# Kernel optimization log

Hardware: AMD Instinct MI355X
Metric: run time of the kernel (lower is better)

## Reference

```python
import jax, jax.numpy as jnp
import numpy as np
import math

N, DIM, HEADS = 4096, 128, 8
HC = DIM // HEADS      # MHA per-head dim = 16
GC = DIM               # TransformerConv per-head out_channels = dim (concat=False)
E = 65536
FFN = 2048
EPS = 1e-5

def layernorm(x, g, b):
    m = x.mean(-1, keepdims=True)
    v = ((x - m) ** 2).mean(-1, keepdims=True)
    return (x - m) * jax.lax.rsqrt(v + EPS) * g + b

def setup_inputs() -> dict:
    key = jax.random.key(0)
    ks = jax.random.split(key, 24)
    s = 0.02
    def nrm(k, shape):
        return jax.random.normal(k, shape, jnp.float32) * s
    return dict(
        x=jax.random.normal(ks[0], (N, DIM), jnp.float32),
        edge_index=jax.random.randint(ks[1], (2, E), 0, N),
        edge_attr=jax.random.normal(ks[2], (E, DIM), jnp.float32),
        n1_g=jnp.ones((DIM,)), n1_b=jnp.zeros((DIM,)),
        n2_g=jnp.ones((DIM,)), n2_b=jnp.zeros((DIM,)),
        n3_g=jnp.ones((DIM,)), n3_b=jnp.zeros((DIM,)),
        w_qkv=nrm(ks[3], (DIM, 3 * DIM)), b_qkv=jnp.zeros((3 * DIM,)),
        w_o=nrm(ks[4], (DIM, DIM)), b_o=jnp.zeros((DIM,)),
        w_query=nrm(ks[5], (DIM, HEADS * GC)), b_query=jnp.zeros((HEADS * GC,)),
        w_key=nrm(ks[6], (DIM, HEADS * GC)), b_key=jnp.zeros((HEADS * GC,)),
        w_value=nrm(ks[7], (DIM, HEADS * GC)), b_value=jnp.zeros((HEADS * GC,)),
        w_edge=nrm(ks[8], (DIM, HEADS * GC)), b_edge=jnp.zeros((HEADS * GC,)),
        w_skip=nrm(ks[9], (DIM, GC)), b_skip=jnp.zeros((GC,)),
        w_beta=nrm(ks[10], (3 * GC, 1)),
        w_f1=nrm(ks[11], (DIM, FFN)), b_f1=jnp.zeros((FFN,)),
        w_f2=nrm(ks[12], (FFN, DIM)), b_f2=jnp.zeros((DIM,)),
        w_dyn=nrm(ks[13], (2 * DIM, DIM)), b_dyn=jnp.zeros((DIM,)),
    )

def reference(x, edge_index, edge_attr, n1_g, n1_b, n2_g, n2_b, n3_g, n3_b,
              w_qkv, b_qkv, w_o, b_o,
              w_query, b_query, w_key, b_key, w_value, b_value,
              w_edge, b_edge, w_skip, b_skip, w_beta,
              w_f1, b_f1, w_f2, b_f2, w_dyn, b_dyn):
    residual = x
    xn = layernorm(x, n1_g, n1_b)
    # ---- dense self-attention (batch 1, batch_first MHA, eval mode) ----
    qkv = xn @ w_qkv + b_qkv
    q, k, v = jnp.split(qkv, 3, axis=-1)
    q = q.reshape(N, HEADS, HC)
    k = k.reshape(N, HEADS, HC)
    v = v.reshape(N, HEADS, HC)
    scores = jnp.einsum('qhd,khd->hqk', q, k) / math.sqrt(HC)
    probs = jax.nn.softmax(scores, axis=-1)
    attn = jnp.einsum('hqk,khd->qhd', probs, v).reshape(N, DIM)
    attn = attn @ w_o + b_o
    x = residual + attn
    # ---- TransformerConv (heads=8, concat=False -> mean, beta=True, edge_dim=dim) ----
    xn2 = layernorm(x, n2_g, n2_b)
    src, dst = edge_index[0], edge_index[1]   # source -> target flow
    qg = (xn2 @ w_query + b_query).reshape(N, HEADS, GC)
    kg = (xn2 @ w_key + b_key).reshape(N, HEADS, GC)
    vg = (xn2 @ w_value + b_value).reshape(N, HEADS, GC)
    eg = (edge_attr @ w_edge + b_edge).reshape(E, HEADS, GC)
    kj = kg[src] + eg                          # key_j + edge embedding
    alpha = jnp.einsum('ehd,ehd->eh', qg[dst], kj) / math.sqrt(GC)  # [E,H]
    amax = jax.ops.segment_max(alpha, dst, num_segments=N)          # [N,H]
    amax = jnp.where(jnp.isfinite(amax), amax, 0.0)
    ea = jnp.exp(alpha - amax[dst])
    denom = jax.ops.segment_sum(ea, dst, num_segments=N)
    w = ea / (denom[dst] + 1e-16)              # segment softmax per target node
    msg = (vg[src] + eg) * w[:, :, None]       # value_j + edge, scaled
    agg = jax.ops.segment_sum(msg, dst, num_segments=N)  # [N,H,GC]
    out = agg.mean(axis=1)                     # concat=False -> head mean
    x_r = xn2 @ w_skip + b_skip                # root/skip path
    beta = jax.nn.sigmoid(jnp.concatenate([out, x_r, out - x_r], axis=-1) @ w_beta)
    graph_out = beta * x_r + (1.0 - beta) * out
    x = x + graph_out
    # ---- FFN ----
    xn3 = layernorm(x, n3_g, n3_b)
    ffn = jax.nn.gelu(xn3 @ w_f1 + b_f1, approximate=False) @ w_f2 + b_f2
    x = x + ffn
    # ---- gated residual fusion ----
    gate = jax.nn.sigmoid(jnp.concatenate([x, residual], axis=-1) @ w_dyn + b_dyn)
    return x * gate + residual * (1.0 - gate)
```

## Files before the change

kernel.cpp:

```cpp
#include <hip/hip_runtime.h>
#include <math.h>
#include <cstddef>

#define NN 4096
#define DIMC 128
#define NHEADS 8
#define NE 65536

typedef unsigned short ushort_t;
typedef short bs8 __attribute__((ext_vector_type(8)));
typedef float f32x16 __attribute__((ext_vector_type(16)));
typedef _Float16 h4 __attribute__((ext_vector_type(4)));
typedef float f4t __attribute__((ext_vector_type(4)));

__device__ __forceinline__ float b2f(ushort_t u){
  unsigned int i = ((unsigned int)u)<<16; float f;
  __builtin_memcpy(&f,&i,4); return f;
}
__device__ __forceinline__ ushort_t f2b(float f){
  unsigned int x; __builtin_memcpy(&x,&f,4);
  unsigned int r = x + 0x7fffu + ((x>>16)&1u);
  return (ushort_t)(r>>16);
}
__device__ __forceinline__ float bdot8(uint4 a, uint4 b){
  unsigned int ua[4]={a.x,a.y,a.z,a.w}, ub[4]={b.x,b.y,b.z,b.w};
  float s=0.f;
  #pragma unroll
  for (int i=0;i<4;++i){
    unsigned int al=ua[i]<<16, ah=ua[i]&0xffff0000u, bl=ub[i]<<16, bh=ub[i]&0xffff0000u;
    float fa,fb,fc,fd;
    __builtin_memcpy(&fa,&al,4); __builtin_memcpy(&fb,&ah,4);
    __builtin_memcpy(&fc,&bl,4); __builtin_memcpy(&fd,&bh,4);
    s += fa*fc + fb*fd;
  }
  return s;
}
__device__ __forceinline__ float bfdot8v(uint4 a, float4 e0, float4 e1){
  unsigned int ua[4]={a.x,a.y,a.z,a.w};
  float eb[8]={e0.x,e0.y,e0.z,e0.w,e1.x,e1.y,e1.z,e1.w};
  float s=0.f;
  #pragma unroll
  for (int i=0;i<4;++i){
    unsigned int al=ua[i]<<16, ah=ua[i]&0xffff0000u;
    float fa,fb;
    __builtin_memcpy(&fa,&al,4); __builtin_memcpy(&fb,&ah,4);
    s += fa*eb[2*i] + fb*eb[2*i+1];
  }
  return s;
}

__global__ __launch_bounds__(128) void ln_kernel(const float* __restrict__ x,
    const float* __restrict__ g, const float* __restrict__ b, ushort_t* __restrict__ y){
  int n = blockIdx.x, d = threadIdx.x;
  __shared__ float red[128];
  float v = x[(size_t)n*DIMC + d];
  red[d] = v; __syncthreads();
  for (int off=64; off>0; off>>=1){ if (d<off) red[d]+=red[d+off]; __syncthreads(); }
  float mean = red[0]*(1.0f/128.0f);
  __syncthreads();
  float c = v-mean;
  red[d] = c*c; __syncthreads();
  for (int off=64; off>0; off>>=1){ if (d<off) red[d]+=red[d+off]; __syncthreads(); }
  float var = red[0]*(1.0f/128.0f);
  y[(size_t)n*DIMC+d] = f2b(c*rsqrtf(var+1e-5f)*g[d]+b[d]);
}

__global__ __launch_bounds__(256) void megawcvt_kernel(
    const float* __restrict__ w_qkv, const float* __restrict__ w_o,
    const float* __restrict__ w_q, const float* __restrict__ w_k,
    const float* __restrict__ w_v, const float* __restrict__ w_e,
    const float* __restrict__ w_f1, const float* __restrict__ w_f2,
    const float* __restrict__ bq, const float* __restrict__ bk,
    const float* __restrict__ w_dyn,
    ushort_t* __restrict__ WBqkv, ushort_t* __restrict__ WBo, ushort_t* __restrict__ WBG,
    ushort_t* __restrict__ WETB, ushort_t* __restrict__ WBf1, ushort_t* __restrict__ WBf2,
    ushort_t* __restrict__ WCAT, float* __restrict__ BCAT, ushort_t* __restrict__ WDYN,
    int* __restrict__ COUNT)
{
  for (int id = blockIdx.x*256+threadIdx.x; id < 1284096; id += gridDim.x*256){
    if (id < 1245184){
      float v; ushort_t* dst; int local;
      if (id < 49152){ local=id; int n=local>>7,k=local&127; v=w_qkv[(size_t)k*384+n]; dst=&WBqkv[local]; }
      else if (id < 65536){ local=id-49152; int n=local>>7,k=local&127; v=w_o[(size_t)k*128+n]; dst=&WBo[local]; }
      else if (id < 327680){ local=id-65536; int n=local>>7,k=local&127;
        v = (n<1024) ? w_q[(size_t)k*1024+n] : w_k[(size_t)k*1024+n-1024];
        dst=&WBG[local]; }
      else if (id < 458752){ local=id-327680; int n=local>>7,k=local&127; v=w_e[(size_t)k*1024+n]; dst=&WETB[local]; }
      else if (id < 720896){ local=id-458752; int n=local>>7,k=local&127; v=w_f1[(size_t)k*2048+n]; dst=&WBf1[local]; }
      else if (id < 983040){ local=id-720896; int n=local>>11,k=local&2047; v=w_f2[(size_t)k*128+n]; dst=&WBf2[local]; }
      else { local=id-983040; int d=local>>11, k=local&2047;
        int h=(k&1023)>>7, i=k&127;
        const float* src = (k<1024) ? w_v : w_e;
        v = src[(size_t)i*1024 + h*128 + d]*0.125f;
        dst=&WCAT[local]; }
      *dst = f2b(v);
    } else if (id < 1247232){
      int local = id - 1245184;
      BCAT[local] = (local<1024) ? bq[local] : bk[local-1024];
    } else if (id < 1280000){
      int local = id - 1247232;
      WDYN[local] = f2b(w_dyn[local]);
    } else {
      COUNT[id-1280000]=0;
    }
  }
}

template<int A_BF16, int C_MODE>
__global__ __launch_bounds__(256) void mgemm_kernel(
    const void* __restrict__ Av, int lda, int strideA,
    const ushort_t* __restrict__ BT, int ldbt, int strideB,
    const float* __restrict__ bias,
    const float* __restrict__ res,
    void* __restrict__ Cv, int ldc, int strideC,
    int K, int act_gelu)
{
  int z = blockIdx.z;
  int m0 = blockIdx.y*128, n0 = blockIdx.x*64;
  int tid = threadIdx.x;
  int w = tid>>6, lane = tid&63;
  int kg = lane>>5;
  int ml = w*32 + (lane&31);
  int sw = (ml>>1)&3;
  __shared__ ushort_t As[128*32];
  const ushort_t* BTz = BT + (size_t)z*strideB;
  f32x16 acc[2];
  #pragma unroll
  for (int i=0;i<16;++i){ acc[0][i]=0.f; acc[1][i]=0.f; }

  for (int k0=0; k0<K; k0+=32){
    {
      int rr = tid>>1, kc = (tid&1)*16;
      int rowg = m0 + rr;
      ushort_t tmp[16] __attribute__((aligned(16)));
      if (A_BF16){
        const ushort_t* A = (const ushort_t*)Av + (size_t)z*strideA;
        uint4 u0 = *(const uint4*)&A[(size_t)rowg*lda + k0 + kc];
        uint4 u1 = *(const uint4*)&A[(size_t)rowg*lda + k0 + kc + 8];
        __builtin_memcpy(tmp, &u0, 16); __builtin_memcpy(tmp+8, &u1, 16);
      } else {
        const float* A = (const float*)Av + (size_t)z*strideA;
        const float* p = &A[(size_t)rowg*lda + k0 + kc];
        float4 f0=*(const float4*)p, f1=*(const float4*)(p+4);
        float4 f2v=*(const float4*)(p+8), f3=*(const float4*)(p+12);
        tmp[0]=f2b(f0.x); tmp[1]=f2b(f0.y); tmp[2]=f2b(f0.z); tmp[3]=f2b(f0.w);
        tmp[4]=f2b(f1.x); tmp[5]=f2b(f1.y); tmp[6]=f2b(f1.z); tmp[7]=f2b(f1.w);
        tmp[8]=f2b(f2v.x); tmp[9]=f2b(f2v.y); tmp[10]=f2b(f2v.z); tmp[11]=f2b(f2v.w);
        tmp[12]=f2b(f3.x); tmp[13]=f2b(f3.y); tmp[14]=f2b(f3.z); tmp[15]=f2b(f3.w);
      }
      int swr = (rr>>1)&3, c0 = kc>>3;
      *(uint4*)&As[rr*32 + (((c0  )^swr)*8)] = *(const uint4*)tmp;
      *(uint4*)&As[rr*32 + (((c0+1)^swr)*8)] = *(const uint4*)(tmp+8);
    }
    __syncthreads();
    bs8 a0 = *(bs8*)&As[ml*32 + (((0*2+kg)^sw)*8)];
    bs8 a1 = *(bs8*)&As[ml*32 + (((1*2+kg)^sw)*8)];
    #pragma unroll
    for (int nt=0; nt<2; ++nt){
      const ushort_t* bp = &BTz[(size_t)(n0 + nt*32 + (lane&31))*ldbt + k0 + kg*8];
      uint4 rb0 = *(const uint4*)bp;
      uint4 rb1 = *(const uint4*)(bp + 16);
      bs8 b0, b1;
      __builtin_memcpy(&b0, &rb0, 16); __builtin_memcpy(&b1, &rb1, 16);
      acc[nt] = __builtin_amdgcn_mfma_f32_32x32x16_bf16(a0, b0, acc[nt], 0,0,0);
      acc[nt] = __builtin_amdgcn_mfma_f32_32x32x16_bf16(a1, b1, acc[nt], 0,0,0);
    }
    __syncthreads();
  }
  #pragma unroll
  for (int nt=0; nt<2; ++nt){
    int col = n0 + nt*32 + (lane&31);
    float bv = bias ? bias[col] : 0.f;
    #pragma unroll
    for (int r=0; r<16; ++r){
      int rowl = (r&3) + 8*(r>>2) + 4*kg;
      int row = m0 + w*32 + rowl;
      float v = acc[nt][r] + bv;
      if (act_gelu) v = 0.5f*v*(1.0f+erff(v*0.70710678118654752f));
      if (res) v += res[(size_t)row*ldc + col];
      size_t idx = (size_t)z*strideC + (size_t)row*ldc + col;
      if (C_MODE==1)      ((ushort_t*)Cv)[idx] = f2b(v);
      else if (C_MODE==2) ((_Float16*)Cv)[idx] = (_Float16)v;
      else                ((float*)Cv)[idx]    = v;
    }
  }
}

__global__ __launch_bounds__(256) void vtrans_kernel(const _Float16* __restrict__ qkvh,
    _Float16* __restrict__ vt){
  int id = blockIdx.x*256+threadIdx.x;
  int n = id & 4095, d = id >> 12;
  vt[(size_t)d*4096 + n] = qkvh[(size_t)n*384 + 256 + d];
}

__global__ __launch_bounds__(256) void flash_kernel(const _Float16* __restrict__ qkvh,
    const _Float16* __restrict__ vt, float* __restrict__ attn){
  int h = blockIdx.y;
  int w = threadIdx.x >> 6, lane = threadIdx.x & 63;
  int q0 = blockIdx.x*64;
  int col = lane & 15, quad = lane >> 4;
  __shared__ float ll[4][4][16];
  __shared__ float lo[4][4][256];
  h4 qf[4];
  #pragma unroll
  for (int t=0;t<4;++t)
    qf[t] = *(const h4*)&qkvh[(size_t)(q0+t*16+col)*384 + h*16 + quad*4];
  f4t ov[4];
  float ls[4] = {0.f,0.f,0.f,0.f};
  #pragma unroll
  for (int t=0;t<4;++t){ ov[t][0]=0.f; ov[t][1]=0.f; ov[t][2]=0.f; ov[t][3]=0.f; }
  const _Float16* kbase = qkvh + 128 + h*16 + quad*4;
  const _Float16* vbase = vt + (size_t)(h*16+col)*4096 + quad*4;
  int jbeg = w*1024, jend = jbeg + 1024;
  h4 kf = *(const h4*)&kbase[(size_t)(jbeg+col)*384];
  h4 vf = *(const h4*)&vbase[jbeg];
  for (int j0=jbeg; j0<jend; j0+=16){
    h4 kc=kf, vc=vf;
    if (j0+16<jend){
      kf = *(const h4*)&kbase[(size_t)(j0+16+col)*384];
      vf = *(const h4*)&vbase[j0+16];
    }
    f4t s[4];
    #pragma unroll
    for (int t=0;t<4;++t){
      s[t][0]=0.f; s[t][1]=0.f; s[t][2]=0.f; s[t][3]=0.f;
      s[t] = __builtin_amdgcn_mfma_f32_16x16x16f16(kc, qf[t], s[t], 0,0,0);
    }
    #pragma unroll
    for (int t=0;t<4;++t){
      float p0=__expf(s[t][0]*0.25f), p1=__expf(s[t][1]*0.25f);
      float p2=__expf(s[t][2]*0.25f), p3=__expf(s[t][3]*0.25f);
      ls[t] += p0+p1+p2+p3;
      h4 pf; pf[0]=(_Float16)p0; pf[1]=(_Float16)p1; pf[2]=(_Float16)p2; pf[3]=(_Float16)p3;
      ov[t] = __builtin_amdgcn_mfma_f32_16x16x16f16(vc, pf, ov[t], 0,0,0);
    }
  }
  #pragma unroll
  for (int t=0;t<4;++t){
    float l = ls[t];
    l += __shfl_xor(l,16);
    l += __shfl_xor(l,32);
    if (lane<16) ll[w][t][lane]=l;
    *(float4*)&lo[w][t][lane*4] = make_float4(ov[t][0],ov[t][1],ov[t][2],ov[t][3]);
  }
  __syncthreads();
  {
    int t = w;
    float l = ll[0][t][col]+ll[1][t][col]+ll[2][t][col]+ll[3][t][col];
    float4 os = make_float4(0.f,0.f,0.f,0.f);
    #pragma unroll
    for (int ww=0; ww<4; ++ww){
      float4 owv = *(const float4*)&lo[ww][t][lane*4];
      os.x += owv.x; os.y += owv.y; os.z += owv.z; os.w += owv.w;
    }
    float inv = 1.0f/l;
    *(float4*)&attn[(size_t)(q0+t*16+col)*128 + h*16 + quad*4] =
        make_float4(os.x*inv, os.y*inv, os.z*inv, os.w*inv);
  }
}

__global__ __launch_bounds__(256) void alpha_kernel(
    const float* __restrict__ ea, const ushort_t* __restrict__ qkvsg,
    const ushort_t* __restrict__ t, const int* __restrict__ csr,
    const int* __restrict__ pack, float* __restrict__ alpha){
  int tid = threadIdx.x;
  int w = tid>>6, lane = tid&63;
  int h = lane>>3, li = lane&7;
  int off = h*128 + li*16;
  int ibase = blockIdx.x*8 + w*2;
  int2 pk = *(const int2*)&pack[ibase];
  int2 ec = *(const int2*)&csr[ibase];
  int e0 = ec.x & (NE-1), e1 = ec.y & (NE-1);
  int s0 = pk.x & 4095, d0 = (pk.x>>12) & 4095;
  int s1 = pk.y & 4095, d1 = (pk.y>>12) & 4095;

  const ushort_t* q0p = &qkvsg[(size_t)d0*2048 + off];
  const ushort_t* k0p = &qkvsg[(size_t)s0*2048 + 1024 + off];
  const ushort_t* t0p = &t[(size_t)d0*1024 + off];
  const float*    e0p = &ea[(size_t)e0*128 + li*16];
  const ushort_t* q1p = &qkvsg[(size_t)d1*2048 + off];
  const ushort_t* k1p = &qkvsg[(size_t)s1*2048 + 1024 + off];
  const ushort_t* t1p = &t[(size_t)d1*1024 + off];
  const float*    e1p = &ea[(size_t)e1*128 + li*16];

  uint4 q00=*(const uint4*)q0p,      q01=*(const uint4*)(q0p+8);
  uint4 k00=*(const uint4*)k0p,      k01=*(const uint4*)(k0p+8);
  uint4 t00=*(const uint4*)t0p,      t01=*(const uint4*)(t0p+8);
  float4 ea00=*(const float4*)e0p,   ea01=*(const float4*)(e0p+4);
  float4 ea02=*(const float4*)(e0p+8), ea03=*(const float4*)(e0p+12);
  uint4 q10=*(const uint4*)q1p,      q11=*(const uint4*)(q1p+8);
  uint4 k10=*(const uint4*)k1p,      k11=*(const uint4*)(k1p+8);
  uint4 t10=*(const uint4*)t1p,      t11=*(const uint4*)(t1p+8);
  float4 ea10=*(const float4*)e1p,   ea11=*(const float4*)(e1p+4);
  float4 ea12=*(const float4*)(e1p+8), ea13=*(const float4*)(e1p+12);

  float p0 = bdot8(q00,k00) + bdot8(q01,k01)
           + bfdot8v(t00,ea00,ea01) + bfdot8v(t01,ea02,ea03);
  float p1 = bdot8(q10,k10) + bdot8(q11,k11)
           + bfdot8v(t10,ea10,ea11) + bfdot8v(t11,ea12,ea13);
  p0 += __shfl_xor(p0,1); p0 += __shfl_xor(p0,2); p0 += __shfl_xor(p0,4);
  p1 += __shfl_xor(p1,1); p1 += __shfl_xor(p1,2); p1 += __shfl_xor(p1,4);
  if (li==0){
    alpha[(size_t)ibase*8 + h]     = 0.08838834764831845f*p0;
    alpha[(size_t)(ibase+1)*8 + h] = 0.08838834764831845f*p1;
  }
}

__global__ __launch_bounds__(256) void count_kernel(const int* __restrict__ ei, int* __restrict__ cnt){
  int e = blockIdx.x*256+threadIdx.x;
  atomicAdd(&cnt[ei[NE+e] & (NN-1)],1);
}
__global__ __launch_bounds__(1024) void scan_kernel(const int* __restrict__ cnt,
    int* __restrict__ rows, int* __restrict__ cursor){
  __shared__ int sums[1024];
  int tid=threadIdx.x;
  int c0=cnt[tid*4], c1=cnt[tid*4+1], c2=cnt[tid*4+2], c3=cnt[tid*4+3];
  int local=c0+c1+c2+c3;
  sums[tid]=local;
  __syncthreads();
  for (int off=1; off<1024; off<<=1){
    int v = (tid>=off)? sums[tid-off] : 0;
    __syncthreads();
    sums[tid]+=v;
    __syncthreads();
  }
  int r = sums[tid]-local;
  rows[tid*4]=r;   cursor[tid*4]=r;   r+=c0;
  rows[tid*4+1]=r; cursor[tid*4+1]=r; r+=c1;
  rows[tid*4+2]=r; cursor[tid*4+2]=r; r+=c2;
  rows[tid*4+3]=r; cursor[tid*4+3]=r; r+=c3;
  if (tid==1023) rows[4096]=r;
}
__global__ __launch_bounds__(256) void scatter_kernel(const int* __restrict__ ei,
    int* __restrict__ cursor, int* __restrict__ csr, int* __restrict__ pack){
  int e = blockIdx.x*256+threadIdx.x;
  int src = ei[e] & (NN-1), dst = ei[NE+e] & (NN-1);
  int pos = atomicAdd(&cursor[dst],1);
  if (pos >= 0 && pos < NE){ csr[pos]=e; pack[pos] = src | (dst<<12); }
}

__global__ __launch_bounds__(256) void agg1_kernel(
    const ushort_t* __restrict__ lns, const float* __restrict__ ea,
    const float* __restrict__ abuf, const int* __restrict__ rows, const int* __restrict__ csr,
    const int* __restrict__ pack,
    const float* __restrict__ b_edge, const float* __restrict__ b_v,
    ushort_t* __restrict__ seagg, float* __restrict__ part)
{
  int n = blockIdx.x, tid = threadIdx.x;
  int d = tid & 127, h0 = tid >> 7;
  float sacc[4]={0.f,0.f,0.f,0.f}, eacc[4]={0.f,0.f,0.f,0.f}, wsacc[4]={0.f,0.f,0.f,0.f};
  float mh[4]={-1e30f,-1e30f,-1e30f,-1e30f};
  float be[4];
  #pragma unroll
  for (int j=0;j<4;++j){
    int hd = (h0+2*j)*128 + d;
    be[j] = b_edge[hd] + b_v[hd];
  }
  int i0=rows[n], i1=rows[n+1];
  i0 = max(0,min(i0,NE)); i1 = max(i0,min(i1,NE));
  for (int i=i0;i<i1;++i){
    #pragma unroll
    for (int j=0;j<4;++j) mh[j] = fmaxf(mh[j], abuf[(size_t)i*8 + h0 + 2*j]);
  }
  __shared__ float smh[8];
  __shared__ float wls[16][8];
  __shared__ int es[16], srcs[16];
  if (d==0){
    #pragma unroll
    for (int j=0;j<4;++j) smh[h0+2*j]=mh[j];
  }
  __syncthreads();
  for (int cs=i0; cs<i1; cs+=16){
    int cnt = min(16, i1-cs);
    if (tid < cnt){
      es[tid]   = csr[cs+tid] & (NE-1);
      srcs[tid] = pack[cs+tid] & (NN-1);
    }
    if (tid < cnt*8){
      int k=tid>>3, hh=tid&7;
      wls[k][hh] = __expf(abuf[(size_t)(cs+k)*8+hh]-smh[hh]);
    }
    __syncthreads();
    for (int k=0;k<cnt;++k){
      int e = es[k], sr = srcs[k];
      float lv = b2f(lns[(size_t)sr*128 + d]);
      float eav = ea[(size_t)e*128 + d];
      #pragma unroll
      for (int j=0;j<4;++j){
        float wv = wls[k][h0+2*j];
        sacc[j] += wv*lv;
        eacc[j] += wv*eav;
        wsacc[j] += wv;
      }
    }
    __syncthreads();
  }
  float partial = 0.f;
  #pragma unroll
  for (int j=0;j<4;++j){
    float inv = 1.0f/(wsacc[j]+1e-16f);
    int hd = (h0+2*j)*128 + d;
    seagg[(size_t)n*2048 + hd]        = f2b(sacc[j]*inv);
    seagg[(size_t)n*2048 + 1024 + hd] = f2b(eacc[j]*inv);
    partial += be[j]*wsacc[j]*inv;
  }
  __shared__ float pp[2][128];
  pp[h0][d] = partial;
  __syncthreads();
  if (tid<128) part[(size_t)n*128+tid] = (pp[0][tid]+pp[1][tid])*0.125f;
}

__global__ __launch_bounds__(128) void combine_kernel(float* __restrict__ x2,
    const float* __restrict__ corrp, const float* __restrict__ part,
    const ushort_t* __restrict__ lns, const float* __restrict__ w_s,
    const float* __restrict__ b_s, const float* __restrict__ x1,
    const float* __restrict__ w_beta)
{
  int n=blockIdx.x, d=threadIdx.x;
  __shared__ float lnrow[128];
  __shared__ float sred[128];
  __shared__ float sbeta;
  size_t idx = (size_t)n*128+d;
  lnrow[d] = b2f(lns[idx]);
  __syncthreads();
  float xrv = b_s[d];
  #pragma unroll 4
  for (int i=0;i<128;++i) xrv += lnrow[i]*w_s[(size_t)i*128+d];
  float o = part[idx] + corrp[idx] + corrp[524288+idx] + corrp[1048576+idx] + corrp[1572864+idx];
  sred[d] = o*w_beta[d] + xrv*w_beta[128+d] + (o-xrv)*w_beta[256+d];
  __syncthreads();
  for (int off=64; off>0; off>>=1){ if (d<off) sred[d]+=sred[d+off]; __syncthreads(); }
  if (d==0) sbeta = 1.0f/(1.0f+__expf(-sred[0]));
  __syncthreads();
  float beta=sbeta;
  x2[idx] = x1[idx] + beta*xrv + (1.0f-beta)*o;
}

__global__ __launch_bounds__(128) void gate_kernel(const float* __restrict__ x3p,
    const float* __restrict__ b_f2, const float* __restrict__ x2,
    const float* __restrict__ x0, const ushort_t* __restrict__ wdyn,
    const float* __restrict__ b_dyn, float* __restrict__ out){
  int n=blockIdx.x, d=threadIdx.x;
  __shared__ float s[256];
  size_t idx = (size_t)n*128+d;
  float a = x3p[idx] + x3p[524288+idx] + x3p[1048576+idx] + x3p[1572864+idx]
          + b_f2[d] + x2[idx];
  float r = x0[idx];
  s[d]=a; s[128+d]=r;
  __syncthreads();
  float g = b_dyn[d];
  for (int k=0;k<256;++k) g += s[k]*b2f(wdyn[(size_t)k*128+d]);
  g = 1.0f/(1.0f+__expf(-g));
  out[idx] = a*g + r*(1.0f-g);
}

extern "C" void kernel_launch(void* const* d_in, const int* in_sizes, int n_in,
                              void* d_out, int out_size, void* d_ws, size_t ws_size,
                              hipStream_t stream) {
  const float* x    =(const float*)d_in[0];
  const int*   ei   =(const int*)  d_in[1];
  const float* eattr=(const float*)d_in[2];
  const float* n1g=(const float*)d_in[3], *n1b=(const float*)d_in[4];
  const float* n2g=(const float*)d_in[5], *n2b=(const float*)d_in[6];
  const float* n3g=(const float*)d_in[7], *n3b=(const float*)d_in[8];
  const float* w_qkv=(const float*)d_in[9],  *b_qkv=(const float*)d_in[10];
  const float* w_o  =(const float*)d_in[11], *b_o  =(const float*)d_in[12];
  const float* w_q  =(const float*)d_in[13], *b_q  =(const float*)d_in[14];
  const float* w_k  =(const float*)d_in[15], *b_k  =(const float*)d_in[16];
  const float* w_v  =(const float*)d_in[17], *b_v  =(const float*)d_in[18];
  const float* w_e  =(const float*)d_in[19], *b_e  =(const float*)d_in[20];
  const float* w_s  =(const float*)d_in[21], *b_s  =(const float*)d_in[22];
  const float* w_beta=(const float*)d_in[23];
  const float* w_f1 =(const float*)d_in[24], *b_f1=(const float*)d_in[25];
  const float* w_f2 =(const float*)d_in[26], *b_f2=(const float*)d_in[27];
  const float* w_dyn=(const float*)d_in[28], *b_dyn=(const float*)d_in[29];
  float* out=(float*)d_out;
  float* ws=(float*)d_ws;

  float* X1    = ws + 0;
  float* X2    = ws + 524288;
  ushort_t* LNS = (ushort_t*)(ws + 1048576);
  float* PART  = ws + 1310720;
  float* ALPHA = ws + 1835008;
  int*   ROWS  = (int*)(ws + 2359296);
  int*   CURS  = (int*)(ws + 2363456);
  int*   CSR   = (int*)(ws + 2367552);
  int*   COUNT = (int*)(ws + 2433088);
  int*   PACK  = (int*)(ws + 524288);
  ushort_t* WBqkv = (ushort_t*)(ws + 2437184);
  ushort_t* WBo   = (ushort_t*)(ws + 2461760);
  ushort_t* WBG   = (ushort_t*)(ws + 2469952);
  ushort_t* WETB  = (ushort_t*)(ws + 2601024);
  ushort_t* WBf1  = (ushort_t*)(ws + 2666560);
  ushort_t* WBf2  = (ushort_t*)(ws + 2797632);
  ushort_t* WCAT  = (ushort_t*)(ws + 2928704);
  float* BCAT  = ws + 3059776;
  ushort_t* WDYN = (ushort_t*)(ws + 3061824);
  _Float16* QKVH  = (_Float16*)(ws + 3078208);
  _Float16* VT    = (_Float16*)(ws + 3864640);
  ushort_t* QKVSG = (ushort_t*)(ws + 3078208);
  ushort_t* SEAGG = (ushort_t*)(ws + 3078208);
  ushort_t* MID   = (ushort_t*)(ws + 3078208);
  ushort_t* T     = (ushort_t*)(ws + 7272512);
  float* CORRP = ws + 7272512;
  float* X3P   = ws + 7272512;
  float* ATTN  = X2;

  megawcvt_kernel<<<2048,256,0,stream>>>(w_qkv,w_o,w_q,w_k,w_v,w_e,w_f1,w_f2,
                                         b_q,b_k,w_dyn,
                                         WBqkv,WBo,WBG,WETB,WBf1,WBf2,WCAT,BCAT,WDYN,COUNT);

  ln_kernel<<<NN,128,0,stream>>>(x, n1g, n1b, LNS);
  mgemm_kernel<1,2><<<dim3(6,32,1),256,0,stream>>>(LNS,128,0, WBqkv,128,0, b_qkv, nullptr, QKVH,384,0, 128, 0);
  vtrans_kernel<<<2048,256,0,stream>>>(QKVH, VT);
  flash_kernel<<<dim3(64,8),256,0,stream>>>(QKVH, VT, ATTN);
  mgemm_kernel<0,0><<<dim3(2,32,1),256,0,stream>>>(ATTN,128,0, WBo,128,0, b_o, x, X1,128,0, 128, 0);

  ln_kernel<<<NN,128,0,stream>>>(X1, n2g, n2b, LNS);
  mgemm_kernel<1,1><<<dim3(32,32,1),256,0,stream>>>(LNS,128,0, WBG,128,0, BCAT, nullptr, QKVSG,2048,0, 128, 0);
  mgemm_kernel<1,1><<<dim3(2,32,8),256,0,stream>>>(QKVSG,2048,128, WETB,128,16384, nullptr, nullptr, T,1024,128, 128, 0);
  count_kernel<<<256,256,0,stream>>>(ei, COUNT);
  scan_kernel<<<1,1024,0,stream>>>(COUNT, ROWS, CURS);
  scatter_kernel<<<256,256,0,stream>>>(ei, CURS, CSR, PACK);
  alpha_kernel<<<8192,256,0,stream>>>(eattr, QKVSG, T, CSR, PACK, ALPHA);
  agg1_kernel<<<NN,256,0,stream>>>(LNS, eattr, ALPHA, ROWS, CSR, PACK, b_e, b_v, SEAGG, PART);
  mgemm_kernel<1,0><<<dim3(2,32,4),256,0,stream>>>(SEAGG,2048,512, WCAT,2048,512, nullptr, nullptr, CORRP,128,524288, 512, 0);
  combine_kernel<<<NN,128,0,stream>>>(X2, CORRP, PART, LNS, w_s, b_s, X1, w_beta);

  ln_kernel<<<NN,128,0,stream>>>(X2, n3g, n3b, LNS);
  mgemm_kernel<1,1><<<dim3(32,32,1),256,0,stream>>>(LNS,128,0, WBf1,128,0, b_f1, nullptr, MID,2048,0, 128, 1);
  mgemm_kernel<1,0><<<dim3(2,32,4),256,0,stream>>>(MID,2048,512, WBf2,2048,512, nullptr, nullptr, X3P,128,524288, 512, 0);

  gate_kernel<<<NN,128,0,stream>>>(X3P, b_f2, X2, x, WDYN, b_dyn, out);
}
```

Measured before the change: 411.2 us.

## Fold softmax scale into Q weights, use exp2, and split flash keys across 8 waves

Pre-multiplies the Q projection weights and bias by the attention scale times log2(e) during weight conversion, so the flash kernel can use the hardware exp2 directly. The flash kernel block grows to 512 threads, with 8 waves each handling 512 keys before a shared-memory reduction. This targets the low occupancy of the attention kernel and removes a multiply per exponential. The trade-off is more shared memory and a larger cross-wave reduction. The scaled bias buffer is stored in a workspace slot that is overwritten later.

After: 399.2 us. 2.9% less time.

```diff
diff --git a/kernel.cpp b/kernel.cpp
--- a/kernel.cpp
+++ b/kernel.cpp
@@ -65,22 +65,25 @@
   y[(size_t)n*DIMC+d] = f2b(c*rsqrtf(var+1e-5f)*g[d]+b[d]);
 }
 
+#define QSCALE 0.36067376022224085f
 __global__ __launch_bounds__(256) void megawcvt_kernel(
     const float* __restrict__ w_qkv, const float* __restrict__ w_o,
     const float* __restrict__ w_q, const float* __restrict__ w_k,
     const float* __restrict__ w_v, const float* __restrict__ w_e,
     const float* __restrict__ w_f1, const float* __restrict__ w_f2,
     const float* __restrict__ bq, const float* __restrict__ bk,
-    const float* __restrict__ w_dyn,
+    const float* __restrict__ w_dyn, const float* __restrict__ b_qkv,
     ushort_t* __restrict__ WBqkv, ushort_t* __restrict__ WBo, ushort_t* __restrict__ WBG,
     ushort_t* __restrict__ WETB, ushort_t* __restrict__ WBf1, ushort_t* __restrict__ WBf2,
     ushort_t* __restrict__ WCAT, float* __restrict__ BCAT, ushort_t* __restrict__ WDYN,
-    int* __restrict__ COUNT)
+    int* __restrict__ COUNT, float* __restrict__ BQKV)
 {
-  for (int id = blockIdx.x*256+threadIdx.x; id < 1284096; id += gridDim.x*256){
+  for (int id = blockIdx.x*256+threadIdx.x; id < 1284480; id += gridDim.x*256){
     if (id < 1245184){
       float v; ushort_t* dst; int local;
-      if (id < 49152){ local=id; int n=local>>7,k=local&127; v=w_qkv[(size_t)k*384+n]; dst=&WBqkv[local]; }
+      if (id < 49152){ local=id; int n=local>>7,k=local&127; v=w_qkv[(size_t)k*384+n];
+        if (n<128) v *= QSCALE;
+        dst=&WBqkv[local]; }
       else if (id < 65536){ local=id-49152; int n=local>>7,k=local&127; v=w_o[(size_t)k*128+n]; dst=&WBo[local]; }
       else if (id < 327680){ local=id-65536; int n=local>>7,k=local&127;
         v = (n<1024) ? w_q[(size_t)k*1024+n] : w_k[(size_t)k*1024+n-1024];
@@ -100,8 +103,11 @@
     } else if (id < 1280000){
       int local = id - 1247232;
       WDYN[local] = f2b(w_dyn[local]);
+    } else if (id < 1284096){
+      COUNT[id-1280000]=0;
     } else {
-      COUNT[id-1280000]=0;
+      int local = id - 1284096;
+      BQKV[local] = b_qkv[local] * ((local<128) ? QSCALE : 1.0f);
     }
   }
 }
@@ -193,14 +199,14 @@
   vt[(size_t)d*4096 + n] = qkvh[(size_t)n*384 + 256 + d];
 }
 
-__global__ __launch_bounds__(256) void flash_kernel(const _Float16* __restrict__ qkvh,
+__global__ __launch_bounds__(512) void flash_kernel(const _Float16* __restrict__ qkvh,
     const _Float16* __restrict__ vt, float* __restrict__ attn){
   int h = blockIdx.y;
   int w = threadIdx.x >> 6, lane = threadIdx.x & 63;
   int q0 = blockIdx.x*64;
   int col = lane & 15, quad = lane >> 4;
-  __shared__ float ll[4][4][16];
-  __shared__ float lo[4][4][256];
+  __shared__ float ll[8][4][16];
+  __shared__ float lo[8][4][256];
   h4 qf[4];
   #pragma unroll
   for (int t=0;t<4;++t)
@@ -211,7 +217,7 @@
   for (int t=0;t<4;++t){ ov[t][0]=0.f; ov[t][1]=0.f; ov[t][2]=0.f; ov[t][3]=0.f; }
   const _Float16* kbase = qkvh + 128 + h*16 + quad*4;
   const _Float16* vbase = vt + (size_t)(h*16+col)*4096 + quad*4;
-  int jbeg = w*1024, jend = jbeg + 1024;
+  int jbeg = w*512, jend = jbeg + 512;
   h4 kf = *(const h4*)&kbase[(size_t)(jbeg+col)*384];
   h4 vf = *(const h4*)&vbase[jbeg];
   for (int j0=jbeg; j0<jend; j0+=16){
@@ -228,9 +234,9 @@
     }
     #pragma unroll
     for (int t=0;t<4;++t){
-      float p0=__expf(s[t][0]*0.25f), p1=__expf(s[t][1]*0.25f);
-      float p2=__expf(s[t][2]*0.25f), p3=__expf(s[t][3]*0.25f);
-      ls[t] += p0+p1+p2+p3;
+      float p0=__builtin_amdgcn_exp2f(s[t][0]), p1=__builtin_amdgcn_exp2f(s[t][1]);
+      float p2=__builtin_amdgcn_exp2f(s[t][2]), p3=__builtin_amdgcn_exp2f(s[t][3]);
+      ls[t] += (p0+p1)+(p2+p3);
       h4 pf; pf[0]=(_Float16)p0; pf[1]=(_Float16)p1; pf[2]=(_Float16)p2; pf[3]=(_Float16)p3;
       ov[t] = __builtin_amdgcn_mfma_f32_16x16x16f16(vc, pf, ov[t], 0,0,0);
     }
@@ -244,12 +250,14 @@
     *(float4*)&lo[w][t][lane*4] = make_float4(ov[t][0],ov[t][1],ov[t][2],ov[t][3]);
   }
   __syncthreads();
-  {
+  if (w < 4){
     int t = w;
-    float l = ll[0][t][col]+ll[1][t][col]+ll[2][t][col]+ll[3][t][col];
+    float l = 0.f;
+    #pragma unroll
+    for (int ww=0; ww<8; ++ww) l += ll[ww][t][col];
     float4 os = make_float4(0.f,0.f,0.f,0.f);
     #pragma unroll
-    for (int ww=0; ww<4; ++ww){
+    for (int ww=0; ww<8; ++ww){
       float4 owv = *(const float4*)&lo[ww][t][lane*4];
       os.x += owv.x; os.y += owv.y; os.z += owv.z; os.w += owv.w;
     }
@@ -487,6 +495,7 @@
   int*   CSR   = (int*)(ws + 2367552);
   int*   COUNT = (int*)(ws + 2433088);
   int*   PACK  = (int*)(ws + 524288);
+  float* BQKV  = ws + 1048576 - 512;
   ushort_t* WBqkv = (ushort_t*)(ws + 2437184);
   ushort_t* WBo   = (ushort_t*)(ws + 2461760);
   ushort_t* WBG   = (ushort_t*)(ws + 2469952);
@@ -507,13 +516,13 @@
   float* ATTN  = X2;
 
   megawcvt_kernel<<<2048,256,0,stream>>>(w_qkv,w_o,w_q,w_k,w_v,w_e,w_f1,w_f2,
-                                         b_q,b_k,w_dyn,
-                                         WBqkv,WBo,WBG,WETB,WBf1,WBf2,WCAT,BCAT,WDYN,COUNT);
+                                         b_q,b_k,w_dyn,b_qkv,
+                                         WBqkv,WBo,WBG,WETB,WBf1,WBf2,WCAT,BCAT,WDYN,COUNT,BQKV);
 
   ln_kernel<<<NN,128,0,stream>>>(x, n1g, n1b, LNS);
-  mgemm_kernel<1,2><<<dim3(6,32,1),256,0,stream>>>(LNS,128,0, WBqkv,128,0, b_qkv, nullptr, QKVH,384,0, 128, 0);
+  mgemm_kernel<1,2><<<dim3(6,32,1),256,0,stream>>>(LNS,128,0, WBqkv,128,0, BQKV, nullptr, QKVH,384,0, 128, 0);
   vtrans_kernel<<<2048,256,0,stream>>>(QKVH, VT);
-  flash_kernel<<<dim3(64,8),256,0,stream>>>(QKVH, VT, ATTN);
+  flash_kernel<<<dim3(64,8),512,0,stream>>>(QKVH, VT, ATTN);
   mgemm_kernel<0,0><<<dim3(2,32,1),256,0,stream>>>(ATTN,128,0, WBo,128,0, b_o, x, X1,128,0, 128, 0);
 
   ln_kernel<<<NN,128,0,stream>>>(X1, n2g, n2b, LNS);
```
